# Optimization experiments

Measured on AMD Instinct MI355X. Metric: run time of the kernel, lower is better.

The kernel has to match this reference:

```python
import jax, jax.numpy as jnp
import numpy as np

SIZE = 256
D_IN = 256
EPS = 1e-3  # keras BatchNormalization default epsilon


def _mlp(x, W1, b1, W2, b2):
    # smallMLP: Dense(size, relu) -> Dense(size)
    return jax.nn.relu(x @ W1 + b1) @ W2 + b2


def setup_inputs() -> dict:
    key = jax.random.key(0)
    ks = jax.random.split(key, 20)
    B, L1, L2 = 16, 1024, 1024
    s = 0.02
    inp = {
        "seq1M": jax.random.normal(ks[0], (B, L1, D_IN), jnp.float32),
        "seq2M": jax.random.normal(ks[1], (B, L2, D_IN), jnp.float32),
        "distogram": jax.random.uniform(ks[2], (B, L1, L2), jnp.float32),
        # shared K/Q/V smallMLP params (same layers applied to seq1 and seq2)
        "kW1": jax.random.normal(ks[3], (D_IN, SIZE), jnp.float32) * s,
        "kb1": jnp.zeros((SIZE,), jnp.float32),
        "kW2": jax.random.normal(ks[4], (SIZE, SIZE), jnp.float32) * s,
        "kb2": jnp.zeros((SIZE,), jnp.float32),
        "qW1": jax.random.normal(ks[5], (D_IN, SIZE), jnp.float32) * s,
        "qb1": jnp.zeros((SIZE,), jnp.float32),
        "qW2": jax.random.normal(ks[6], (SIZE, SIZE), jnp.float32) * s,
        "qb2": jnp.zeros((SIZE,), jnp.float32),
        "vW1": jax.random.normal(ks[7], (D_IN, SIZE), jnp.float32) * s,
        "vb1": jnp.zeros((SIZE,), jnp.float32),
        "vW2": jax.random.normal(ks[8], (SIZE, SIZE), jnp.float32) * s,
        "vb2": jnp.zeros((SIZE,), jnp.float32),
        # output projections
        "fc1W": jax.random.normal(ks[9], (SIZE, SIZE), jnp.float32) * s,
        "fc1b": jnp.zeros((SIZE,), jnp.float32),
        "fc2W": jax.random.normal(ks[10], (SIZE, SIZE), jnp.float32) * s,
        "fc2b": jnp.zeros((SIZE,), jnp.float32),
        # shared BatchNorm (inference mode, moving stats)
        "bn_gamma": jnp.ones((SIZE,), jnp.float32),
        "bn_beta": jnp.zeros((SIZE,), jnp.float32),
        "bn_mean": jnp.zeros((SIZE,), jnp.float32),
        "bn_var": jnp.ones((SIZE,), jnp.float32),
    }
    return inp


def reference(seq1M, seq2M, distogram,
              kW1, kb1, kW2, kb2,
              qW1, qb1, qW2, qb2,
              vW1, vb1, vW2, vb2,
              fc1W, fc1b, fc2W, fc2b,
              bn_gamma, bn_beta, bn_mean, bn_var):
    size = jnp.float32(SIZE)
    k1 = _mlp(seq1M, kW1, kb1, kW2, kb2)   # [B, L1, S]
    q1 = _mlp(seq1M, qW1, qb1, qW2, qb2)
    v1 = _mlp(seq1M, vW1, vb1, vW2, vb2)
    k2 = _mlp(seq2M, kW1, kb1, kW2, kb2)   # [B, L2, S]
    q2 = _mlp(seq2M, qW1, qb1, qW2, qb2)
    v2 = _mlp(seq2M, vW1, vb1, vW2, vb2)

    # distogram-scaled scores, softmax over axis 1 (query axis — non-standard)
    scores1 = jnp.einsum('bls,bms->blm', q1, k2) * distogram / size  # [B, L1, L2]
    w1 = jax.nn.softmax(scores1, axis=1)
    scores2 = jnp.einsum('bms,bls->bml', q2, k1) * jnp.transpose(distogram, (0, 2, 1)) / size  # [B, L2, L1]
    w2 = jax.nn.softmax(scores2, axis=1)

    # transpose(matmul(V^T, W), [0,2,1]) == einsum contracting the softmax axis
    ap1 = jnp.einsum('bls,blm->bms', v1, w1)  # [B, L2, S]
    ap2 = jnp.einsum('bms,bml->bls', v2, w2)  # [B, L1, S]

    def bn(x):
        return (x - bn_mean) * jax.lax.rsqrt(bn_var + EPS) * bn_gamma + bn_beta

    out1 = bn(jax.nn.relu(ap1 @ fc1W + fc1b))
    out2 = bn(jax.nn.relu(ap2 @ fc2W + fc2b))
    return out1, out2
```

## Files before the change

### kernel.cpp

```cpp
#include <hip/hip_runtime.h>
#include <hip/hip_bf16.h>


typedef __attribute__((ext_vector_type(8))) short bf16x8;
typedef __attribute__((ext_vector_type(4))) float f32x4;
typedef unsigned short u16;

__device__ __forceinline__ unsigned int f2bfbits(float f) {
  union { float f; unsigned int i; } v; v.f = f;
  return (v.i + 0x7fffu + ((v.i >> 16) & 1u)) >> 16;
}
__device__ __forceinline__ unsigned int pk2(float a, float b) {
  return f2bfbits(a) | (f2bfbits(b) << 16);
}
__device__ __forceinline__ float bf2f(u16 x) {
  union { unsigned int i; float f; } v;
  v.i = (unsigned int)x << 16;
  return v.f;
}

__global__ void pack_wt(const float* __restrict__ w0, const float* __restrict__ w1,
                        const float* __restrict__ w2, const float* __restrict__ w3,
                        const float* __restrict__ w4, const float* __restrict__ w5,
                        const float* __restrict__ w6, const float* __restrict__ w7,
                        u16* __restrict__ out) {
  const float* wsel[8] = {w0, w1, w2, w3, w4, w5, w6, w7};
  const float* W = wsel[blockIdx.y];
  u16* o = out + (size_t)blockIdx.y * 65536;
  int i0 = blockIdx.x * 1024 + threadIdx.x * 4;
  int n = i0 >> 8, k = i0 & 255;
  float a = W[(k + 0) * 256 + n];
  float b = W[(k + 1) * 256 + n];
  float c = W[(k + 2) * 256 + n];
  float d = W[(k + 3) * 256 + n];
  uint2 pv;
  pv.x = pk2(a, b);
  pv.y = pk2(c, d);
  *(uint2*)(o + i0) = pv;
}

__global__ __launch_bounds__(256)
void pack_disto(const float* __restrict__ D, u16* __restrict__ Dt) {
  __shared__ u16 T[64][72];
  const int b = blockIdx.z, l0 = blockIdx.y * 64, m0 = blockIdx.x * 64;
  const float* src = D + (size_t)b * (1024 * 1024);
  u16* dst = Dt + (size_t)b * (1024 * 1024);
  const int r = threadIdx.x >> 2, c0 = (threadIdx.x & 3) * 16;
  float4 f[4];
#pragma unroll
  for (int q = 0; q < 4; ++q)
    f[q] = *(const float4*)(src + (size_t)(l0 + r) * 1024 + m0 + c0 + q * 4);
  uint4 p0, p1;
  p0.x = pk2(f[0].x, f[0].y); p0.y = pk2(f[0].z, f[0].w);
  p0.z = pk2(f[1].x, f[1].y); p0.w = pk2(f[1].z, f[1].w);
  p1.x = pk2(f[2].x, f[2].y); p1.y = pk2(f[2].z, f[2].w);
  p1.z = pk2(f[3].x, f[3].y); p1.w = pk2(f[3].z, f[3].w);
  *(uint4*)&T[r][c0] = p0;
  *(uint4*)&T[r][c0 + 8] = p1;
  __syncthreads();
  u16 vals[16];
#pragma unroll
  for (int k = 0; k < 16; ++k) vals[k] = T[c0 + k][r];
  *(uint4*)(dst + (size_t)(m0 + r) * 1024 + l0 + c0) = *(uint4*)&vals[0];
  *(uint4*)(dst + (size_t)(m0 + r) * 1024 + l0 + c0 + 8) = *(uint4*)&vals[8];
}

__global__ __launch_bounds__(256, 2)
void mlp3_fused(const float* __restrict__ seqA, const float* __restrict__ seqB,
                const u16* __restrict__ Wt8,
                const float* __restrict__ kb1, const float* __restrict__ kb2,
                const float* __restrict__ qb1, const float* __restrict__ qb2,
                const float* __restrict__ vb1, const float* __restrict__ vb2,
                u16* __restrict__ kA, u16* __restrict__ qA, u16* __restrict__ vA,
                u16* __restrict__ kB, u16* __restrict__ qB, u16* __restrict__ vB)
{
  __shared__ u16 As[64][256];
  __shared__ u16 Hl[64][256];

  const int tid = threadIdx.x;
  const int lane = tid & 63;
  const int w = tid >> 6;
  const int l15 = lane & 15, lq = lane >> 4;
  const int seqsel = blockIdx.x >> 8;
  const size_t m0 = (size_t)(blockIdx.x & 255) * 64;
  const float* __restrict__ seq = seqsel ? seqB : seqA;

  {
    const int row = tid >> 2, cg = tid & 3;
    const float* src = seq + (m0 + row) * 256 + cg * 64;
#pragma unroll
    for (int cc = 0; cc < 8; ++cc) {
      float4 f0 = *(const float4*)(src + cc * 8);
      float4 f1 = *(const float4*)(src + cc * 8 + 4);
      uint4 pk;
      pk.x = pk2(f0.x, f0.y);
      pk.y = pk2(f0.z, f0.w);
      pk.z = pk2(f1.x, f1.y);
      pk.w = pk2(f1.z, f1.w);
      const int ch = (cg * 8 + cc) ^ (row & 7);
      *(uint4*)&As[row][ch * 8] = pk;
    }
  }
  __syncthreads();

  for (int mlp = 0; mlp < 3; ++mlp) {
    const u16* __restrict__ W1 = Wt8 + (size_t)(mlp * 2) * 65536;
    const u16* __restrict__ W2 = W1 + 65536;
    const float* __restrict__ b1 = (mlp == 0) ? kb1 : (mlp == 1) ? qb1 : vb1;
    const float* __restrict__ b2 = (mlp == 0) ? kb2 : (mlp == 1) ? qb2 : vb2;
    u16* __restrict__ dst =
        (mlp == 0) ? (seqsel ? kB : kA) : (mlp == 1) ? (seqsel ? qB : qA) : (seqsel ? vB : vA);

    const u16* __restrict__ w1b = W1 + (size_t)(w * 64 + l15) * 256 + lq * 8;
    const u16* __restrict__ w2b = W2 + (size_t)(w * 64 + l15) * 256 + lq * 8;

    bf16x8 wf[4];
#pragma unroll
    for (int ni = 0; ni < 4; ++ni) wf[ni] = *(const bf16x8*)(w1b + ni * 4096);

    float b1v[4][4];
#pragma unroll
    for (int ni = 0; ni < 4; ++ni)
#pragma unroll
      for (int r = 0; r < 4; ++r) b1v[ni][r] = b1[w * 64 + ni * 16 + 4 * lq + r];
    float b2v[4];
#pragma unroll
    for (int ni = 0; ni < 4; ++ni) b2v[ni] = b2[w * 64 + ni * 16 + l15];

    f32x4 a1[4][4];
#pragma unroll
    for (int ni = 0; ni < 4; ++ni)
#pragma unroll
      for (int mj = 0; mj < 4; ++mj) a1[ni][mj] = (f32x4)0.0f;
#pragma unroll
    for (int ks = 0; ks < 8; ++ks) {
      bf16x8 wn[4];
      if (ks < 7) {
#pragma unroll
        for (int ni = 0; ni < 4; ++ni)
          wn[ni] = *(const bf16x8*)(w1b + ni * 4096 + (ks + 1) * 32);
      }
      bf16x8 af[4];
#pragma unroll
      for (int mj = 0; mj < 4; ++mj) {
        const int row = mj * 16 + l15;
        const int ch = (ks * 4 + lq) ^ (row & 7);
        af[mj] = *(const bf16x8*)&As[row][ch * 8];
      }
#pragma unroll
      for (int ni = 0; ni < 4; ++ni)
#pragma unroll
        for (int mj = 0; mj < 4; ++mj)
          a1[ni][mj] = __builtin_amdgcn_mfma_f32_16x16x32_bf16(wf[ni], af[mj], a1[ni][mj], 0, 0, 0);
#pragma unroll
      for (int ni = 0; ni < 4; ++ni) wf[ni] = wn[ni];
    }

    __syncthreads();

#pragma unroll
    for (int ni = 0; ni < 4; ++ni) wf[ni] = *(const bf16x8*)(w2b + ni * 4096);

#pragma unroll
    for (int ni = 0; ni < 4; ++ni) {
      const int chl = w * 8 + ni * 2 + (lq >> 1);
#pragma unroll
      for (int mj = 0; mj < 4; ++mj) {
        const int m = mj * 16 + l15;
        float h0 = fmaxf(a1[ni][mj][0] + b1v[ni][0], 0.f);
        float h1 = fmaxf(a1[ni][mj][1] + b1v[ni][1], 0.f);
        float h2 = fmaxf(a1[ni][mj][2] + b1v[ni][2], 0.f);
        float h3 = fmaxf(a1[ni][mj][3] + b1v[ni][3], 0.f);
        uint2 pv;
        pv.x = pk2(h0, h1);
        pv.y = pk2(h2, h3);
        const int ch = chl ^ (m & 7);
        *(uint2*)&Hl[m][ch * 8 + (lq & 1) * 4] = pv;
      }
    }
    __syncthreads();

    f32x4 a2[4][4];
#pragma unroll
    for (int mi = 0; mi < 4; ++mi)
#pragma unroll
      for (int ni = 0; ni < 4; ++ni) a2[mi][ni] = (f32x4)0.0f;
#pragma unroll
    for (int ks = 0; ks < 8; ++ks) {
      bf16x8 wn[4];
      if (ks < 7) {
#pragma unroll
        for (int ni = 0; ni < 4; ++ni)
          wn[ni] = *(const bf16x8*)(w2b + ni * 4096 + (ks + 1) * 32);
      }
      bf16x8 hf[4];
#pragma unroll
      for (int mi = 0; mi < 4; ++mi) {
        const int row = mi * 16 + l15;
        const int ch = (ks * 4 + lq) ^ (row & 7);
        hf[mi] = *(const bf16x8*)&Hl[row][ch * 8];
      }
#pragma unroll
      for (int mi = 0; mi < 4; ++mi)
#pragma unroll
        for (int ni = 0; ni < 4; ++ni)
          a2[mi][ni] = __builtin_amdgcn_mfma_f32_16x16x32_bf16(hf[mi], wf[ni], a2[mi][ni], 0, 0, 0);
#pragma unroll
      for (int ni = 0; ni < 4; ++ni) wf[ni] = wn[ni];
    }

#pragma unroll
    for (int ni = 0; ni < 4; ++ni) {
      const int col = w * 64 + ni * 16 + l15;
      const float bb = b2v[ni];
#pragma unroll
      for (int mi = 0; mi < 4; ++mi) {
        const size_t grow0 = m0 + mi * 16 + 4 * lq;
        float z[4];
#pragma unroll
        for (int r = 0; r < 4; ++r) z[r] = a2[mi][ni][r] + bb;
        if (mlp != 2) {
#pragma unroll
          for (int r = 0; r < 4; ++r)
            dst[(grow0 + r) * 256 + col] = (u16)f2bfbits(z[r]);
        } else {
          uint2 pv;
          pv.x = pk2(z[0], z[1]);
          pv.y = pk2(z[2], z[3]);
          const size_t bb2 = grow0 >> 10, lrow = grow0 & 1023;
          *(uint2*)(dst + ((size_t)bb2 * 256 + col) * 1024 + lrow) = pv;
        }
      }
    }
  }
}

enum { EPI_RELU_BF16 = 0, EPI_BF16 = 1, EPI_VT = 2, EPI_BN = 3 };

template <bool AF32, int EPI>
__global__ __launch_bounds__(256, 2)
void gemm_mfma(const void* __restrict__ Aptr, const u16* __restrict__ Wt,
               const float* __restrict__ bias, void* __restrict__ Cout,
               const float* __restrict__ bn_g, const float* __restrict__ bn_b,
               const float* __restrict__ bn_m, const float* __restrict__ bn_v)
{
  __shared__ u16 As[128][64];
  __shared__ u16 Ws[64][64];
  const int tid = threadIdx.x;
  const int lane = tid & 63;
  const int w = tid >> 6;
  const int wr = w >> 1, wc = w & 1;
  const int l15 = lane & 15, lq = lane >> 4;
  const size_t bm = (size_t)blockIdx.x * 128;
  const int bn = blockIdx.y * 64;

  const int sar = tid >> 1, sah = tid & 1;
  const int swr = tid >> 2, swc = tid & 3;

  f32x4 acc[4][2];
#pragma unroll
  for (int mi = 0; mi < 4; ++mi)
#pragma unroll
    for (int ni = 0; ni < 2; ++ni) acc[mi][ni] = (f32x4)0.0f;

  for (int k0 = 0; k0 < 256; k0 += 64) {
    __syncthreads();
    if (AF32) {
      const float* A = (const float*)Aptr + (bm + sar) * 256 + k0 + sah * 32;
#pragma unroll
      for (int c = 0; c < 4; ++c) {
        float4 f0 = *(const float4*)(A + c * 8);
        float4 f1 = *(const float4*)(A + c * 8 + 4);
        uint4 pk;
        pk.x = pk2(f0.x, f0.y);
        pk.y = pk2(f0.z, f0.w);
        pk.z = pk2(f1.x, f1.y);
        pk.w = pk2(f1.z, f1.w);
        int cc = (sah * 4 + c) ^ (sar & 7);
        *(uint4*)&As[sar][cc * 8] = pk;
      }
    } else {
      const u16* A = (const u16*)Aptr + (bm + sar) * 256 + k0 + sah * 32;
#pragma unroll
      for (int c = 0; c < 4; ++c) {
        uint4 v = *(const uint4*)(A + c * 8);
        int cc = (sah * 4 + c) ^ (sar & 7);
        *(uint4*)&As[sar][cc * 8] = v;
      }
    }
    {
      const u16* Wp = Wt + (size_t)(bn + swr) * 256 + k0 + swc * 16;
#pragma unroll
      for (int c = 0; c < 2; ++c) {
        uint4 v = *(const uint4*)(Wp + c * 8);
        int cc = (swc * 2 + c) ^ (swr & 7);
        *(uint4*)&Ws[swr][cc * 8] = v;
      }
    }
    __syncthreads();
#pragma unroll
    for (int ks = 0; ks < 2; ++ks) {
      bf16x8 af[4], wf[2];
#pragma unroll
      for (int mi = 0; mi < 4; ++mi) {
        int row = wr * 64 + mi * 16 + l15;
        int cc = (ks * 4 + lq) ^ (row & 7);
        af[mi] = *(const bf16x8*)&As[row][cc * 8];
      }
#pragma unroll
      for (int ni = 0; ni < 2; ++ni) {
        int row = wc * 32 + ni * 16 + l15;
        int cc = (ks * 4 + lq) ^ (row & 7);
        wf[ni] = *(const bf16x8*)&Ws[row][cc * 8];
      }
#pragma unroll
      for (int mi = 0; mi < 4; ++mi)
#pragma unroll
        for (int ni = 0; ni < 2; ++ni)
          acc[mi][ni] = __builtin_amdgcn_mfma_f32_16x16x32_bf16(
              af[mi], wf[ni], acc[mi][ni], 0, 0, 0);
    }
  }

#pragma unroll
  for (int ni = 0; ni < 2; ++ni) {
    const int col = bn + wc * 32 + ni * 16 + l15;
    const float bi = bias[col];
    float g = 0.f, be = 0.f, mu = 0.f, iv = 0.f;
    if (EPI == EPI_BN) {
      g = bn_g[col];
      be = bn_b[col];
      mu = bn_m[col];
      iv = rsqrtf(bn_v[col] + 1e-3f);
    }
#pragma unroll
    for (int mi = 0; mi < 4; ++mi) {
      const size_t grow0 = bm + wr * 64 + mi * 16 + 4 * lq;
      float z[4];
#pragma unroll
      for (int r = 0; r < 4; ++r) z[r] = acc[mi][ni][r] + bi;
      if (EPI == EPI_RELU_BF16) {
#pragma unroll
        for (int r = 0; r < 4; ++r)
          ((u16*)Cout)[(grow0 + r) * 256 + col] = (u16)f2bfbits(fmaxf(z[r], 0.f));
      } else if (EPI == EPI_BF16) {
#pragma unroll
        for (int r = 0; r < 4; ++r)
          ((u16*)Cout)[(grow0 + r) * 256 + col] = (u16)f2bfbits(z[r]);
      } else if (EPI == EPI_VT) {
        uint2 pv;
        pv.x = pk2(z[0], z[1]);
        pv.y = pk2(z[2], z[3]);
        const size_t b = grow0 >> 10, lrow = grow0 & 1023;
        *(uint2*)((u16*)Cout + ((size_t)b * 256 + col) * 1024 + lrow) = pv;
      } else {
#pragma unroll
        for (int r = 0; r < 4; ++r) {
          float zz = fmaxf(z[r], 0.f);
          ((float*)Cout)[(grow0 + r) * 256 + col] = (zz - mu) * iv * g + be;
        }
      }
    }
  }
}

__global__ __launch_bounds__(256, 2)
void attn_mfma(const u16* __restrict__ Qa, const u16* __restrict__ Ka,
               const u16* __restrict__ Va, u16* __restrict__ OutA,
               const u16* __restrict__ Qb, const u16* __restrict__ Kb,
               const u16* __restrict__ Vb, u16* __restrict__ OutB,
               const u16* __restrict__ D1t, const float* __restrict__ D2)
{
  __shared__ union U {
    struct {
      u16 Ks[2][32][256];
      u16 Vts[256][32];
      u16 Pl[64][40];
    } s;
    u16 Osw[4][16][264];
  } u;

  const int orig = blockIdx.x;
  const int lid = (orig & 7) * 64 + (orig >> 3);
  const int dir = lid >> 8;
  const int b = (lid >> 4) & 15;
  const int i0 = (lid & 15) * 64;

  const u16* __restrict__ Q = dir ? Qb : Qa;
  const u16* __restrict__ K = dir ? Kb : Ka;
  const u16* __restrict__ Vt = dir ? Vb : Va;
  u16* __restrict__ Out = dir ? OutB : OutA;

  const int tid = threadIdx.x;
  const int lane = tid & 63;
  const int w = tid >> 6;
  const int l15 = lane & 15, lq = lane >> 4;
  const size_t sbase = (size_t)b * (1024 * 256);
  const size_t vtbase = (size_t)b * (256 * 1024);
  const size_t dbase = (size_t)b * (1024 * 1024);

  bf16x8 q[8];
  {
    const u16* Qp = Q + sbase + (size_t)(i0 + w * 16 + l15) * 256 + lq * 8;
#pragma unroll
    for (int ks = 0; ks < 8; ++ks) q[ks] = *(const bf16x8*)(Qp + ks * 32);
  }

  const int cb0 = w * 4;
  auto stage_K = [&](int bi, int j0) {
#pragma unroll
    for (int i = 0; i < 4; ++i) {
      const int cb = cb0 + i;
      const int krow = cb * 2 + (lane >> 5);
      const int kch = (lane & 31) ^ (krow & 7);
      const u16* gs = K + sbase + (size_t)(j0 + krow) * 256 + kch * 8;
      __builtin_amdgcn_global_load_lds(
          (const __attribute__((address_space(1))) unsigned int*)gs,
          (__attribute__((address_space(3))) unsigned int*)&u.s.Ks[bi][cb * 2][0],
          16, 0, 0);
    }
  };
  auto stage_V = [&](int j0) {
#pragma unroll
    for (int i = 0; i < 4; ++i) {
      const int cb = cb0 + i;
      const int vrow = cb * 16 + (lane >> 2);
      const int vch = lane & 3;
      const u16* gs = Vt + vtbase + (size_t)vrow * 1024 + j0 + ((vch ^ (vrow & 3)) * 8);
      __builtin_amdgcn_global_load_lds(
          (const __attribute__((address_space(1))) unsigned int*)gs,
          (__attribute__((address_space(3))) unsigned int*)&u.s.Vts[cb * 16][0],
          16, 0, 0);
    }
  };

  float mrow[4], lsum[4];
  f32x4 o[16];
#pragma unroll
  for (int r = 0; r < 4; ++r) { mrow[r] = -1e30f; lsum[r] = 0.f; }
#pragma unroll
  for (int nt = 0; nt < 16; ++nt) o[nt] = (f32x4)0.0f;

  stage_K(0, 0);

  const int vcc = lq ^ (l15 & 3);

  for (int t = 0; t < 32; ++t) {
    const int bi = t & 1;
    const int j0 = t * 32;

    u16 bregu[8];
    float bregf[8];
    if (dir == 0) {
#pragma unroll
      for (int nt = 0; nt < 2; ++nt)
#pragma unroll
        for (int r = 0; r < 4; ++r)
          bregu[nt * 4 + r] =
              D1t[dbase + (size_t)(i0 + w * 16 + 4 * lq + r) * 1024 + j0 + l15 + 16 * nt];
    } else {
#pragma unroll
      for (int nt = 0; nt < 2; ++nt)
#pragma unroll
        for (int r = 0; r < 4; ++r)
          bregf[nt * 4 + r] =
              D2[dbase + (size_t)(i0 + w * 16 + 4 * lq + r) * 1024 + j0 + l15 + 16 * nt];
    }

    stage_V(j0);
    __builtin_amdgcn_sched_barrier(0);
    if (t + 1 < 32) {
      stage_K(bi ^ 1, j0 + 32);
      asm volatile("s_waitcnt vmcnt(16)" ::: "memory");
    } else {
      asm volatile("s_waitcnt vmcnt(12)" ::: "memory");
    }
    __builtin_amdgcn_s_barrier();
    __builtin_amdgcn_sched_barrier(0);

    f32x4 sa[2];
    sa[0] = (f32x4)0.0f;
    sa[1] = (f32x4)0.0f;
    __builtin_amdgcn_s_setprio(1);
#pragma unroll
    for (int ks = 0; ks < 8; ++ks)
#pragma unroll
      for (int nt = 0; nt < 2; ++nt) {
        const int row = nt * 16 + l15;
        const int cc = (ks * 4 + lq) ^ (row & 7);
        bf16x8 kb = *(const bf16x8*)&u.s.Ks[bi][row][cc * 8];
        sa[nt] = __builtin_amdgcn_mfma_f32_16x16x32_bf16(q[ks], kb, sa[nt], 0, 0, 0);
      }
    __builtin_amdgcn_s_setprio(0);

    float s0[4], s1[4];
    bool need = false;
#pragma unroll
    for (int r = 0; r < 4; ++r) {
      const float b0 = (dir == 0) ? bf2f(bregu[r]) : bregf[r];
      const float b1 = (dir == 0) ? bf2f(bregu[4 + r]) : bregf[4 + r];
      s0[r] = sa[0][r] * b0 * 0.00390625f;
      s1[r] = sa[1][r] * b1 * 0.00390625f;
      need = need || (s0[r] > mrow[r] + 8.f) || (s1[r] > mrow[r] + 8.f);
    }
    if (__any(need)) {
#pragma unroll
      for (int r = 0; r < 4; ++r) {
        float mx = fmaxf(s0[r], s1[r]);
        mx = fmaxf(mx, __shfl_xor(mx, 1, 16));
        mx = fmaxf(mx, __shfl_xor(mx, 2, 16));
        mx = fmaxf(mx, __shfl_xor(mx, 4, 16));
        mx = fmaxf(mx, __shfl_xor(mx, 8, 16));
        const float mn = fmaxf(mrow[r], mx);
        const float sc = __expf(mrow[r] - mn);
        mrow[r] = mn;
        lsum[r] *= sc;
#pragma unroll
        for (int nt = 0; nt < 16; ++nt) o[nt][r] *= sc;
      }
    }
    float p0v[4], p1v[4];
#pragma unroll
    for (int r = 0; r < 4; ++r) {
      p0v[r] = __expf(s0[r] - mrow[r]);
      p1v[r] = __expf(s1[r] - mrow[r]);
      lsum[r] += p0v[r] + p1v[r];
    }
#pragma unroll
    for (int r = 0; r < 4; ++r) {
      const int qrow = w * 16 + 4 * lq + r;
      u.s.Pl[qrow][l15] = (u16)f2bfbits(p0v[r]);
      u.s.Pl[qrow][16 + l15] = (u16)f2bfbits(p1v[r]);
    }
    if (t + 1 < 32)
      asm volatile("s_waitcnt vmcnt(4) lgkmcnt(0)" ::: "memory");
    else
      asm volatile("s_waitcnt vmcnt(0) lgkmcnt(0)" ::: "memory");
    __builtin_amdgcn_sched_barrier(0);
    __builtin_amdgcn_s_barrier();
    const bf16x8 pa = *(const bf16x8*)&u.s.Pl[w * 16 + l15][lq * 8];

    __builtin_amdgcn_s_setprio(1);
#pragma unroll
    for (int nt = 0; nt < 16; ++nt) {
      bf16x8 vb = *(const bf16x8*)&u.s.Vts[nt * 16 + l15][vcc * 8];
      o[nt] = __builtin_amdgcn_mfma_f32_16x16x32_bf16(pa, vb, o[nt], 0, 0, 0);
    }
    __builtin_amdgcn_s_setprio(0);

    asm volatile("s_waitcnt lgkmcnt(0)" ::: "memory");
    __builtin_amdgcn_s_barrier();
  }

  float inv[4];
#pragma unroll
  for (int r = 0; r < 4; ++r) {
    float rs = lsum[r];
    rs += __shfl_xor(rs, 1, 16);
    rs += __shfl_xor(rs, 2, 16);
    rs += __shfl_xor(rs, 4, 16);
    rs += __shfl_xor(rs, 8, 16);
    inv[r] = 1.0f / rs;
  }
#pragma unroll
  for (int nt = 0; nt < 16; ++nt) {
#pragma unroll
    for (int r = 0; r < 4; ++r)
      u.Osw[w][4 * lq + r][nt * 16 + l15] = (u16)f2bfbits(o[nt][r] * inv[r]);
  }
  asm volatile("s_waitcnt lgkmcnt(0)" ::: "memory");
  __builtin_amdgcn_sched_barrier(0);
  {
    const int orow = lane >> 2, och = (lane & 3) * 64;
    const u16* src = &u.Osw[w][orow][och];
    u16* dst = Out + sbase + (size_t)(i0 + w * 16 + orow) * 256 + och;
#pragma unroll
    for (int c = 0; c < 8; ++c) *(uint4*)(dst + c * 8) = *(const uint4*)(src + c * 8);
  }
}

extern "C" void kernel_launch(void* const* d_in, const int* in_sizes, int n_in,
                              void* d_out, int out_size, void* d_ws, size_t ws_size,
                              hipStream_t stream)
{
  (void)in_sizes; (void)n_in; (void)out_size; (void)ws_size;

  const float* seq1  = (const float*)d_in[0];
  const float* seq2  = (const float*)d_in[1];
  const float* disto = (const float*)d_in[2];
  const float* kW1 = (const float*)d_in[3];
  const float* kb1 = (const float*)d_in[4];
  const float* kW2 = (const float*)d_in[5];
  const float* kb2 = (const float*)d_in[6];
  const float* qW1 = (const float*)d_in[7];
  const float* qb1 = (const float*)d_in[8];
  const float* qW2 = (const float*)d_in[9];
  const float* qb2 = (const float*)d_in[10];
  const float* vW1 = (const float*)d_in[11];
  const float* vb1 = (const float*)d_in[12];
  const float* vW2 = (const float*)d_in[13];
  const float* vb2 = (const float*)d_in[14];
  const float* fc1W = (const float*)d_in[15];
  const float* fc1b = (const float*)d_in[16];
  const float* fc2W = (const float*)d_in[17];
  const float* fc2b = (const float*)d_in[18];
  const float* bn_g = (const float*)d_in[19];
  const float* bn_b = (const float*)d_in[20];
  const float* bn_m = (const float*)d_in[21];
  const float* bn_v = (const float*)d_in[22];

  char* ws = (char*)d_ws;
  const size_t MB = 1024 * 1024;
  u16* Wt8 = (u16*)(ws);
  u16* k1  = (u16*)(ws + 1 * MB);
  u16* q1  = (u16*)(ws + 9 * MB);
  u16* k2  = (u16*)(ws + 17 * MB);
  u16* q2  = (u16*)(ws + 25 * MB);
  u16* v1t = (u16*)(ws + 33 * MB);
  u16* v2t = (u16*)(ws + 41 * MB);
  u16* ap1 = (u16*)(ws + 49 * MB);
  u16* ap2 = (u16*)(ws + 57 * MB);
  u16* D1t = (u16*)(ws + 65 * MB);

  pack_wt<<<dim3(64, 8), 256, 0, stream>>>(kW1, kW2, qW1, qW2, vW1, vW2, fc1W, fc2W, Wt8);
  pack_disto<<<dim3(16, 16, 16), 256, 0, stream>>>(disto, D1t);

  mlp3_fused<<<dim3(512), dim3(256), 0, stream>>>(
      seq1, seq2, Wt8, kb1, kb2, qb1, qb2, vb1, vb2,
      k1, q1, v1t, k2, q2, v2t);

  attn_mfma<<<dim3(512), dim3(256), 0, stream>>>(
      k2, q1, v1t, ap1,
      k1, q2, v2t, ap2,
      D1t, disto);

  float* out1 = (float*)d_out;
  float* out2 = (float*)d_out + 4194304;
  dim3 ggrid(128, 4), gblk(256);
  gemm_mfma<false, EPI_BN><<<ggrid, gblk, 0, stream>>>(
      ap1, Wt8 + 6ull * 65536, fc1b, (void*)out1, bn_g, bn_b, bn_m, bn_v);
  gemm_mfma<false, EPI_BN><<<ggrid, gblk, 0, stream>>>(
      ap2, Wt8 + 7ull * 65536, fc2b, (void*)out2, bn_g, bn_b, bn_m, bn_v);
}
```

Baseline: 173.3 us.

## Double-buffer V tiles, prefetch alongside K, and split QK accumulator chains

V is now double-buffered in LDS and its next tile is prefetched together with the next K tile, rather than loaded at the start of each iteration. That lets the mid-iteration vmcnt wait and block barrier before the PV MFMAs go, since each wave reads back only its own P rows. The QK^T accumulation is split into two independent MFMA chains to shorten the dependent accumulate chain. LDS use grows by 16 KB per block, which may limit occupancy at two blocks per CU.

Result: no change. 175.4 us (+1.2%).

```diff
diff --git a/kernel.cpp b/kernel.cpp
--- a/kernel.cpp
+++ b/kernel.cpp
@@ -374,7 +374,7 @@
   __shared__ union U {
     struct {
       u16 Ks[2][32][256];
-      u16 Vts[256][32];
+      u16 Vts[2][256][32];
       u16 Pl[64][40];
     } s;
     u16 Osw[4][16][264];
@@ -420,7 +420,7 @@
           16, 0, 0);
     }
   };
-  auto stage_V = [&](int j0) {
+  auto stage_V = [&](int bi, int j0) {
 #pragma unroll
     for (int i = 0; i < 4; ++i) {
       const int cb = cb0 + i;
@@ -429,7 +429,7 @@
       const u16* gs = Vt + vtbase + (size_t)vrow * 1024 + j0 + ((vch ^ (vrow & 3)) * 8);
       __builtin_amdgcn_global_load_lds(
           (const __attribute__((address_space(1))) unsigned int*)gs,
-          (__attribute__((address_space(3))) unsigned int*)&u.s.Vts[cb * 16][0],
+          (__attribute__((address_space(3))) unsigned int*)&u.s.Vts[bi][cb * 16][0],
           16, 0, 0);
     }
   };
@@ -442,6 +442,7 @@
   for (int nt = 0; nt < 16; ++nt) o[nt] = (f32x4)0.0f;
 
   stage_K(0, 0);
+  stage_V(0, 0);
 
   const int vcc = lq ^ (l15 & 3);
 
@@ -467,20 +468,21 @@
               D2[dbase + (size_t)(i0 + w * 16 + 4 * lq + r) * 1024 + j0 + l15 + 16 * nt];
     }
 
-    stage_V(j0);
-    __builtin_amdgcn_sched_barrier(0);
     if (t + 1 < 32) {
+      stage_V(bi ^ 1, j0 + 32);
       stage_K(bi ^ 1, j0 + 32);
       asm volatile("s_waitcnt vmcnt(16)" ::: "memory");
     } else {
-      asm volatile("s_waitcnt vmcnt(12)" ::: "memory");
+      asm volatile("s_waitcnt vmcnt(8)" ::: "memory");
     }
     __builtin_amdgcn_s_barrier();
     __builtin_amdgcn_sched_barrier(0);
 
-    f32x4 sa[2];
-    sa[0] = (f32x4)0.0f;
-    sa[1] = (f32x4)0.0f;
+    f32x4 sa[2][2];
+    sa[0][0] = (f32x4)0.0f;
+    sa[0][1] = (f32x4)0.0f;
+    sa[1][0] = (f32x4)0.0f;
+    sa[1][1] = (f32x4)0.0f;
     __builtin_amdgcn_s_setprio(1);
 #pragma unroll
     for (int ks = 0; ks < 8; ++ks)
@@ -489,7 +491,8 @@
         const int row = nt * 16 + l15;
         const int cc = (ks * 4 + lq) ^ (row & 7);
         bf16x8 kb = *(const bf16x8*)&u.s.Ks[bi][row][cc * 8];
-        sa[nt] = __builtin_amdgcn_mfma_f32_16x16x32_bf16(q[ks], kb, sa[nt], 0, 0, 0);
+        sa[nt][ks & 1] =
+            __builtin_amdgcn_mfma_f32_16x16x32_bf16(q[ks], kb, sa[nt][ks & 1], 0, 0, 0);
       }
     __builtin_amdgcn_s_setprio(0);
 
@@ -499,8 +502,8 @@
     for (int r = 0; r < 4; ++r) {
       const float b0 = (dir == 0) ? bf2f(bregu[r]) : bregf[r];
       const float b1 = (dir == 0) ? bf2f(bregu[4 + r]) : bregf[4 + r];
-      s0[r] = sa[0][r] * b0 * 0.00390625f;
-      s1[r] = sa[1][r] * b1 * 0.00390625f;
+      s0[r] = (sa[0][0][r] + sa[0][1][r]) * b0 * 0.00390625f;
+      s1[r] = (sa[1][0][r] + sa[1][1][r]) * b1 * 0.00390625f;
       need = need || (s0[r] > mrow[r] + 8.f) || (s1[r] > mrow[r] + 8.f);
     }
     if (__any(need)) {
@@ -532,18 +535,14 @@
       u.s.Pl[qrow][l15] = (u16)f2bfbits(p0v[r]);
       u.s.Pl[qrow][16 + l15] = (u16)f2bfbits(p1v[r]);
     }
-    if (t + 1 < 32)
-      asm volatile("s_waitcnt vmcnt(4) lgkmcnt(0)" ::: "memory");
-    else
-      asm volatile("s_waitcnt vmcnt(0) lgkmcnt(0)" ::: "memory");
+    asm volatile("s_waitcnt lgkmcnt(0)" ::: "memory");
     __builtin_amdgcn_sched_barrier(0);
-    __builtin_amdgcn_s_barrier();
     const bf16x8 pa = *(const bf16x8*)&u.s.Pl[w * 16 + l15][lq * 8];
 
     __builtin_amdgcn_s_setprio(1);
 #pragma unroll
     for (int nt = 0; nt < 16; ++nt) {
-      bf16x8 vb = *(const bf16x8*)&u.s.Vts[nt * 16 + l15][vcc * 8];
+      bf16x8 vb = *(const bf16x8*)&u.s.Vts[bi][nt * 16 + l15][vcc * 8];
       o[nt] = __builtin_amdgcn_mfma_f32_16x16x32_bf16(pa, vb, o[nt], 0, 0, 0);
     }
     __builtin_amdgcn_s_setprio(0);
```
